# Kernel optimization log

Measured on AMD Instinct MI355X. Metric: run time of the kernel, lower is better.

Reference implementation:

```python
import jax, jax.numpy as jnp
import numpy as np

N_NODES = 100000
N_EDGES = 1600000
IN_DIM = 256
OUT_DIM = 64


def setup_inputs() -> dict:
    key = jax.random.key(0)
    k1, k2, k3 = jax.random.split(key, 3)
    inputs = jax.random.normal(k1, (N_NODES, IN_DIM), dtype=jnp.float32)
    edge_index = jax.random.randint(k2, (2, N_EDGES), 0, N_NODES, dtype=jnp.int64)
    # Xavier-uniform weight as in nn.init.xavier_uniform_
    limit = float(np.sqrt(6.0 / (IN_DIM + OUT_DIM)))
    weight = jax.random.uniform(k3, (IN_DIM, OUT_DIM), minval=-limit, maxval=limit, dtype=jnp.float32)
    return {"inputs": inputs, "edge_index": edge_index, "weight": weight}


def reference(inputs, edge_index, weight):
    # Dense projection: [N, out_dim]
    x = inputs @ weight
    # Sparse adjacency matmul: out[r] = sum_{(r,c) in edges} x[c]
    rows, cols = edge_index[0], edge_index[1]
    agg = jax.ops.segment_sum(x[cols], rows, num_segments=inputs.shape[0])
    return jax.nn.sigmoid(agg)
```

## Files before the change

### kernel.cpp

```cpp
#include <hip/hip_runtime.h>
#include <hip/hip_fp16.h>
#include <math.h>

#define N_NODES 100000
#define N_EDGES 1600000
#define IN_DIM 256
#define OUT_DIM 64

#define NB 256
#define RPB 391
#define BCAP 6912
#define CAP 32
#define CHUNK_E 2048
#define NBIN_BLK ((N_EDGES + CHUNK_E - 1) / CHUNK_E)

#define X_OFF         0UL
#define WIMG_OFF      25600000UL
#define OFFSETS_OFF   26000000UL
#define BCUR_OFF      26400016UL
#define SORTED_OFF    26801088UL

typedef short bf16x8 __attribute__((ext_vector_type(8)));
typedef float f32x4 __attribute__((ext_vector_type(4)));

__global__ __launch_bounds__(256) void convert_weight(const float* __restrict__ w,
                                                      ushort* __restrict__ img) {
    const int g = blockIdx.x * 256 + threadIdx.x;
    const int j = g & 7, l = (g >> 3) & 63, ts = g >> 9;
    const int s = ts & 7, t = ts >> 3;
    const int k = s * 32 + (l >> 4) * 8 + j;
    const int c = t * 16 + (l & 15);
    const float v = w[k * OUT_DIM + c];
    const unsigned b = __float_as_uint(v);
    const float r = v - __uint_as_float(b & 0xFFFF0000u);
    img[(ts * 2 + 0) * 512 + l * 8 + j] = (ushort)(b >> 16);
    img[(ts * 2 + 1) * 512 + l * 8 + j] = (ushort)(__float_as_uint(r) >> 16);
}

__global__ __launch_bounds__(256) void gemm_mfma(const float* __restrict__ inputs,
                                                 const ushort* __restrict__ wimg,
                                                 __half* __restrict__ x) {
    __shared__ ushort lds[32768];
    const int tid = threadIdx.x;

    #pragma unroll
    for (int i = 0; i < 16; ++i) {
        const int c = tid + i * 256;
        *(int4*)(lds + c * 8) = *(const int4*)(wimg + c * 8);
    }
    __syncthreads();

    const int wv = tid >> 6, l = tid & 63;
    const int rbase = blockIdx.x * 64 + wv * 16;
    const int arow_idx = rbase + (l & 15);
    const int row_c = arow_idx < N_NODES ? arow_idx : N_NODES - 1;
    const float* arow = inputs + (size_t)row_c * IN_DIM;
    const int koff = (l >> 4) * 8;

    bf16x8 ah[8], al[8];
    #pragma unroll
    for (int s = 0; s < 8; ++s) {
        const float4 p = *(const float4*)(arow + s * 32 + koff);
        const float4 q = *(const float4*)(arow + s * 32 + koff + 4);
        const float v[8] = {p.x, p.y, p.z, p.w, q.x, q.y, q.z, q.w};
        #pragma unroll
        for (int j = 0; j < 8; ++j) {
            const unsigned b = __float_as_uint(v[j]);
            const float r = v[j] - __uint_as_float(b & 0xFFFF0000u);
            ah[s][j] = (short)(b >> 16);
            al[s][j] = (short)(__float_as_uint(r) >> 16);
        }
    }

    f32x4 acc[4];
    #pragma unroll
    for (int t = 0; t < 4; ++t) acc[t] = (f32x4){0.f, 0.f, 0.f, 0.f};

    const bf16x8* b8 = (const bf16x8*)lds;
    #pragma unroll
    for (int t = 0; t < 4; ++t) {
        #pragma unroll
        for (int s = 0; s < 8; ++s) {
            const bf16x8 bh = b8[((t * 8 + s) * 2 + 0) * 64 + l];
            const bf16x8 blo = b8[((t * 8 + s) * 2 + 1) * 64 + l];
            acc[t] = __builtin_amdgcn_mfma_f32_16x16x32_bf16(ah[s], bh, acc[t], 0, 0, 0);
            acc[t] = __builtin_amdgcn_mfma_f32_16x16x32_bf16(al[s], bh, acc[t], 0, 0, 0);
            acc[t] = __builtin_amdgcn_mfma_f32_16x16x32_bf16(ah[s], blo, acc[t], 0, 0, 0);
        }
    }

    const int mbase = rbase + (l >> 4) * 4;
    #pragma unroll
    for (int reg = 0; reg < 4; ++reg) {
        const int row = mbase + reg;
        if (row < N_NODES) {
            #pragma unroll
            for (int t = 0; t < 4; ++t)
                x[(size_t)row * OUT_DIM + t * 16 + (l & 15)] = __float2half(acc[t][reg]);
        }
    }
}

__global__ __launch_bounds__(256) void bin_kernel(const int* __restrict__ rows,
                                                  const int* __restrict__ cols,
                                                  int* __restrict__ bcur,
                                                  int* __restrict__ bp) {
    __shared__ int lbuf[NB * CAP];
    __shared__ int lcnt[NB], ltot[NB], lbase[NB];
    const int tid = threadIdx.x;
    lcnt[tid] = 0;
    __syncthreads();

    const int base = blockIdx.x * CHUNK_E;
    #pragma unroll
    for (int g = 0; g < 2; ++g) {
        const int e = base + (g * 256 + tid) * 4;
        if (e < N_EDGES) {
            const int4 r4 = *(const int4*)(rows + e);
            const int4 c4 = *(const int4*)(cols + e);
            const int rr[4] = {r4.x, r4.y, r4.z, r4.w};
            const int cc[4] = {c4.x, c4.y, c4.z, c4.w};
            #pragma unroll
            for (int u = 0; u < 4; ++u) {
                const int r = rr[u];
                const int b = r / RPB;
                const int pack = ((r - b * RPB) << 17) | cc[u];
                const int p = atomicAdd(&lcnt[b], 1);
                if (p < CAP) {
                    lbuf[b * CAP + p] = pack;
                } else {
                    const int gp = atomicAdd(&bcur[b], 1);
                    bp[b * BCAP + gp] = pack;
                }
            }
        }
    }
    __syncthreads();
    {
        const int tot = min(lcnt[tid], CAP);
        ltot[tid] = tot;
        lbase[tid] = atomicAdd(&bcur[tid], tot);
    }
    __syncthreads();
    #pragma unroll
    for (int k = 0; k < 32; ++k) {
        const int b = (k << 3) + (tid >> 5);
        const int i = tid & 31;
        if (i < ltot[b]) bp[b * BCAP + lbase[b] + i] = lbuf[b * CAP + i];
    }
}

__global__ __launch_bounds__(256) void sort_kernel(const int* __restrict__ bp,
                                                   const int* __restrict__ bcur,
                                                   int* __restrict__ offsets,
                                                   int* __restrict__ sorted_cols) {
    __shared__ int ebuf[BCAP];
    __shared__ int sa[256], sb2[256];
    __shared__ int hist[512];
    __shared__ int cur[RPB + 1];
    const int b = blockIdx.x, t = threadIdx.x;

    sa[t] = bcur[t];
    hist[t] = 0; hist[t + 256] = 0;
    __syncthreads();

    int* src = sa; int* dst = sb2;
    for (int off = 1; off < 256; off <<= 1) {
        const int v = src[t] + ((t >= off) ? src[t - off] : 0);
        dst[t] = v; __syncthreads();
        int* tmp = src; src = dst; dst = tmp;
    }
    const int n = bcur[b];
    const int gbase = src[b] - n;
    const int bb = b * BCAP;

    int i = t;
    for (; i + 768 < n; i += 1024) {
        const int v0 = bp[bb + i], v1 = bp[bb + i + 256];
        const int v2 = bp[bb + i + 512], v3 = bp[bb + i + 768];
        ebuf[i] = v0; ebuf[i + 256] = v1; ebuf[i + 512] = v2; ebuf[i + 768] = v3;
        atomicAdd(&hist[v0 >> 17], 1);
        atomicAdd(&hist[v1 >> 17], 1);
        atomicAdd(&hist[v2 >> 17], 1);
        atomicAdd(&hist[v3 >> 17], 1);
    }
    for (; i < n; i += 256) {
        const int v = bp[bb + i];
        ebuf[i] = v;
        atomicAdd(&hist[v >> 17], 1);
    }
    __syncthreads();

    const int h0 = hist[2 * t], h1 = hist[2 * t + 1];
    const int sum2 = h0 + h1;
    sa[t] = sum2; __syncthreads();
    src = sa; dst = sb2;
    for (int off = 1; off < 256; off <<= 1) {
        const int v = src[t] + ((t >= off) ? src[t - off] : 0);
        dst[t] = v; __syncthreads();
        int* tmp = src; src = dst; dst = tmp;
    }
    const int S = src[t];
    const int e0 = 2 * t, e1 = 2 * t + 1;
    const int x0 = S - sum2;
    const int x1 = S - h1;
    if (e0 < RPB) {
        cur[e0] = x0;
        const int row = b * RPB + e0;
        if (row <= N_NODES) offsets[row] = gbase + x0;
    }
    if (e1 < RPB) {
        cur[e1] = x1;
        const int row = b * RPB + e1;
        if (row <= N_NODES) offsets[row] = gbase + x1;
    }
    __syncthreads();

    i = t;
    for (; i + 768 < n; i += 1024) {
        const int v0 = ebuf[i], v1 = ebuf[i + 256], v2 = ebuf[i + 512], v3 = ebuf[i + 768];
        const int p0 = atomicAdd(&cur[v0 >> 17], 1);
        const int p1 = atomicAdd(&cur[v1 >> 17], 1);
        const int p2 = atomicAdd(&cur[v2 >> 17], 1);
        const int p3 = atomicAdd(&cur[v3 >> 17], 1);
        sorted_cols[gbase + p0] = v0 & 0x1FFFF;
        sorted_cols[gbase + p1] = v1 & 0x1FFFF;
        sorted_cols[gbase + p2] = v2 & 0x1FFFF;
        sorted_cols[gbase + p3] = v3 & 0x1FFFF;
    }
    for (; i < n; i += 256) {
        const int v = ebuf[i];
        const int p = atomicAdd(&cur[v >> 17], 1);
        sorted_cols[gbase + p] = v & 0x1FFFF;
    }
}

__global__ __launch_bounds__(256) void aggregate_kernel(const int* __restrict__ offsets,
                                                        const int* __restrict__ sorted_cols,
                                                        const __half* __restrict__ x,
                                                        float* __restrict__ out) {
    const int row = blockIdx.x * 4 + (threadIdx.x >> 6);
    const int lane = threadIdx.x & 63;
    if (row >= N_NODES) return;
    const int start = offsets[row];
    const int end = offsets[row + 1];
    float acc = 0.f;
    int j = start;
    for (; j + 7 < end; j += 8) {
        int c[8];
        #pragma unroll
        for (int u = 0; u < 8; ++u) c[u] = sorted_cols[j + u];
        float a[8];
        #pragma unroll
        for (int u = 0; u < 8; ++u) a[u] = __half2float(x[(size_t)c[u] * OUT_DIM + lane]);
        acc += ((a[0] + a[1]) + (a[2] + a[3])) + ((a[4] + a[5]) + (a[6] + a[7]));
    }
    for (; j < end; ++j)
        acc += __half2float(x[(size_t)sorted_cols[j] * OUT_DIM + lane]);
    out[(size_t)row * OUT_DIM + lane] = 1.f / (1.f + __expf(-acc));
}

extern "C" void kernel_launch(void* const* d_in, const int* in_sizes, int n_in,
                              void* d_out, int out_size, void* d_ws, size_t ws_size,
                              hipStream_t stream) {
    const float* inputs = (const float*)d_in[0];
    const int* edge_index = (const int*)d_in[1];
    const float* weight = (const float*)d_in[2];
    float* out = (float*)d_out;

    char* ws = (char*)d_ws;
    __half* x        = (__half*)(ws + X_OFF);
    int* bp          = (int*)(ws + X_OFF);
    ushort* wimg     = (ushort*)(ws + WIMG_OFF);
    int* offsets     = (int*)(ws + OFFSETS_OFF);
    int* bcur        = (int*)(ws + BCUR_OFF);
    int* sorted_cols = (int*)(ws + SORTED_OFF);

    const int* rows = edge_index;
    const int* cols = edge_index + N_EDGES;

    hipMemsetAsync(bcur, 0, NB * sizeof(int), stream);

    bin_kernel<<<NBIN_BLK, 256, 0, stream>>>(rows, cols, bcur, bp);
    sort_kernel<<<NB, 256, 0, stream>>>(bp, bcur, offsets, sorted_cols);

    convert_weight<<<64, 256, 0, stream>>>(weight, wimg);
    gemm_mfma<<<(N_NODES + 63) / 64, 256, 0, stream>>>(inputs, wimg, x);

    aggregate_kernel<<<(N_NODES + 3) / 4, 256, 0, stream>>>(offsets, sorted_cols, x, out);
}
```

Before: 275.0 us.

## Drop per-row sort and aggregate bucketed edges with shared-memory atomics

Removes the counting-sort kernel and the CSR offsets. The aggregation now launches one block per row bucket. Each block gathers x rows for its bucket's edges and accumulates them into a shared-memory tile with float atomics, then applies the sigmoid and writes out with vector stores. Buckets are halved in size (512 buckets of 196 rows) and each bin block handles twice as many edges. This saves a full kernel launch and a pass over the edge list, at the cost of only 512 aggregation blocks with large LDS footprints and contended LDS atomics, which may cut the latency hiding for the random gathers.

```diff
diff --git a/kernel.cpp b/kernel.cpp
--- a/kernel.cpp
+++ b/kernel.cpp
@@ -7,18 +7,17 @@
 #define IN_DIM 256
 #define OUT_DIM 64
 
-#define NB 256
-#define RPB 391
-#define BCAP 6912
-#define CAP 32
-#define CHUNK_E 2048
+#define NB 512
+#define RPB 196
+#define BCAP 3712
+#define CAP 24
+#define CHUNK_E 4096
 #define NBIN_BLK ((N_EDGES + CHUNK_E - 1) / CHUNK_E)
 
 #define X_OFF         0UL
-#define WIMG_OFF      25600000UL
-#define OFFSETS_OFF   26000000UL
-#define BCUR_OFF      26400016UL
-#define SORTED_OFF    26801088UL
+#define BP_OFF        12800000UL
+#define WIMG_OFF      20500000UL
+#define BCUR_OFF      20600000UL
 
 typedef short bf16x8 __attribute__((ext_vector_type(8)));
 typedef float f32x4 __attribute__((ext_vector_type(4)));
@@ -108,12 +107,12 @@
     __shared__ int lbuf[NB * CAP];
     __shared__ int lcnt[NB], ltot[NB], lbase[NB];
     const int tid = threadIdx.x;
-    lcnt[tid] = 0;
+    lcnt[tid] = 0; lcnt[tid + 256] = 0;
     __syncthreads();
 
     const int base = blockIdx.x * CHUNK_E;
     #pragma unroll
-    for (int g = 0; g < 2; ++g) {
+    for (int g = 0; g < 4; ++g) {
         const int e = base + (g * 256 + tid) * 4;
         if (e < N_EDGES) {
             const int4 r4 = *(const int4*)(rows + e);
@@ -136,128 +135,65 @@
         }
     }
     __syncthreads();
-    {
-        const int tot = min(lcnt[tid], CAP);
-        ltot[tid] = tot;
-        lbase[tid] = atomicAdd(&bcur[tid], tot);
-    }
-    __syncthreads();
-    #pragma unroll
-    for (int k = 0; k < 32; ++k) {
+    #pragma unroll
+    for (int q = 0; q < 2; ++q) {
+        const int b = tid + q * 256;
+        const int tot = min(lcnt[b], CAP);
+        ltot[b] = tot;
+        lbase[b] = atomicAdd(&bcur[b], tot);
+    }
+    __syncthreads();
+    #pragma unroll
+    for (int k = 0; k < 64; ++k) {
         const int b = (k << 3) + (tid >> 5);
         const int i = tid & 31;
         if (i < ltot[b]) bp[b * BCAP + lbase[b] + i] = lbuf[b * CAP + i];
     }
 }
 
-__global__ __launch_bounds__(256) void sort_kernel(const int* __restrict__ bp,
-                                                   const int* __restrict__ bcur,
-                                                   int* __restrict__ offsets,
-                                                   int* __restrict__ sorted_cols) {
-    __shared__ int ebuf[BCAP];
-    __shared__ int sa[256], sb2[256];
-    __shared__ int hist[512];
-    __shared__ int cur[RPB + 1];
-    const int b = blockIdx.x, t = threadIdx.x;
-
-    sa[t] = bcur[t];
-    hist[t] = 0; hist[t + 256] = 0;
-    __syncthreads();
-
-    int* src = sa; int* dst = sb2;
-    for (int off = 1; off < 256; off <<= 1) {
-        const int v = src[t] + ((t >= off) ? src[t - off] : 0);
-        dst[t] = v; __syncthreads();
-        int* tmp = src; src = dst; dst = tmp;
-    }
-    const int n = bcur[b];
-    const int gbase = src[b] - n;
-    const int bb = b * BCAP;
-
-    int i = t;
-    for (; i + 768 < n; i += 1024) {
-        const int v0 = bp[bb + i], v1 = bp[bb + i + 256];
-        const int v2 = bp[bb + i + 512], v3 = bp[bb + i + 768];
-        ebuf[i] = v0; ebuf[i + 256] = v1; ebuf[i + 512] = v2; ebuf[i + 768] = v3;
-        atomicAdd(&hist[v0 >> 17], 1);
-        atomicAdd(&hist[v1 >> 17], 1);
-        atomicAdd(&hist[v2 >> 17], 1);
-        atomicAdd(&hist[v3 >> 17], 1);
-    }
-    for (; i < n; i += 256) {
-        const int v = bp[bb + i];
-        ebuf[i] = v;
-        atomicAdd(&hist[v >> 17], 1);
-    }
-    __syncthreads();
-
-    const int h0 = hist[2 * t], h1 = hist[2 * t + 1];
-    const int sum2 = h0 + h1;
-    sa[t] = sum2; __syncthreads();
-    src = sa; dst = sb2;
-    for (int off = 1; off < 256; off <<= 1) {
-        const int v = src[t] + ((t >= off) ? src[t - off] : 0);
-        dst[t] = v; __syncthreads();
-        int* tmp = src; src = dst; dst = tmp;
-    }
-    const int S = src[t];
-    const int e0 = 2 * t, e1 = 2 * t + 1;
-    const int x0 = S - sum2;
-    const int x1 = S - h1;
-    if (e0 < RPB) {
-        cur[e0] = x0;
-        const int row = b * RPB + e0;
-        if (row <= N_NODES) offsets[row] = gbase + x0;
-    }
-    if (e1 < RPB) {
-        cur[e1] = x1;
-        const int row = b * RPB + e1;
-        if (row <= N_NODES) offsets[row] = gbase + x1;
-    }
-    __syncthreads();
-
-    i = t;
-    for (; i + 768 < n; i += 1024) {
-        const int v0 = ebuf[i], v1 = ebuf[i + 256], v2 = ebuf[i + 512], v3 = ebuf[i + 768];
-        const int p0 = atomicAdd(&cur[v0 >> 17], 1);
-        const int p1 = atomicAdd(&cur[v1 >> 17], 1);
-        const int p2 = atomicAdd(&cur[v2 >> 17], 1);
-        const int p3 = atomicAdd(&cur[v3 >> 17], 1);
-        sorted_cols[gbase + p0] = v0 & 0x1FFFF;
-        sorted_cols[gbase + p1] = v1 & 0x1FFFF;
-        sorted_cols[gbase + p2] = v2 & 0x1FFFF;
-        sorted_cols[gbase + p3] = v3 & 0x1FFFF;
-    }
-    for (; i < n; i += 256) {
-        const int v = ebuf[i];
-        const int p = atomicAdd(&cur[v >> 17], 1);
-        sorted_cols[gbase + p] = v & 0x1FFFF;
-    }
-}
-
-__global__ __launch_bounds__(256) void aggregate_kernel(const int* __restrict__ offsets,
-                                                        const int* __restrict__ sorted_cols,
+__global__ __launch_bounds__(256) void aggregate_kernel(const int* __restrict__ bp,
+                                                        const int* __restrict__ bcur,
                                                         const __half* __restrict__ x,
                                                         float* __restrict__ out) {
-    const int row = blockIdx.x * 4 + (threadIdx.x >> 6);
-    const int lane = threadIdx.x & 63;
-    if (row >= N_NODES) return;
-    const int start = offsets[row];
-    const int end = offsets[row + 1];
-    float acc = 0.f;
-    int j = start;
-    for (; j + 7 < end; j += 8) {
-        int c[8];
+    __shared__ float acc[RPB * OUT_DIM];
+    const int b = blockIdx.x, tid = threadIdx.x;
+    const int w = tid >> 6, lane = tid & 63;
+
+    f32x4* a4 = (f32x4*)acc;
+    for (int i = tid; i < RPB * OUT_DIM / 4; i += 256) a4[i] = (f32x4){0.f, 0.f, 0.f, 0.f};
+    __syncthreads();
+
+    const int n = bcur[b];
+    const unsigned* bb = (const unsigned*)(bp + b * BCAP);
+
+    for (int j0 = w * 8; j0 < n; j0 += 32) {
         #pragma unroll
-        for (int u = 0; u < 8; ++u) c[u] = sorted_cols[j + u];
-        float a[8];
-        #pragma unroll
-        for (int u = 0; u < 8; ++u) a[u] = __half2float(x[(size_t)c[u] * OUT_DIM + lane]);
-        acc += ((a[0] + a[1]) + (a[2] + a[3])) + ((a[4] + a[5]) + (a[6] + a[7]));
-    }
-    for (; j < end; ++j)
-        acc += __half2float(x[(size_t)sorted_cols[j] * OUT_DIM + lane]);
-    out[(size_t)row * OUT_DIM + lane] = 1.f / (1.f + __expf(-acc));
+        for (int u = 0; u < 8; ++u) {
+            const int j = j0 + u;
+            if (j < n) {
+                const unsigned p = bb[j];
+                const int col = p & 0x1FFFF;
+                const int rl = p >> 17;
+                const float v = __half2float(x[(size_t)col * OUT_DIM + lane]);
+                atomicAdd(&acc[rl * OUT_DIM + lane], v);
+            }
+        }
+    }
+    __syncthreads();
+
+    for (int i = tid; i < RPB * (OUT_DIM / 4); i += 256) {
+        const int rr = i >> 4, q = i & 15;
+        const int row = b * RPB + rr;
+        if (row < N_NODES) {
+            const float* ap = acc + rr * OUT_DIM + q * 4;
+            float4 o;
+            o.x = 1.f / (1.f + __expf(-ap[0]));
+            o.y = 1.f / (1.f + __expf(-ap[1]));
+            o.z = 1.f / (1.f + __expf(-ap[2]));
+            o.w = 1.f / (1.f + __expf(-ap[3]));
+            *(float4*)(out + (size_t)row * OUT_DIM + q * 4) = o;
+        }
+    }
 }
 
 extern "C" void kernel_launch(void* const* d_in, const int* in_sizes, int n_in,
@@ -270,11 +206,9 @@
 
     char* ws = (char*)d_ws;
     __half* x        = (__half*)(ws + X_OFF);
-    int* bp          = (int*)(ws + X_OFF);
+    int* bp          = (int*)(ws + BP_OFF);
     ushort* wimg     = (ushort*)(ws + WIMG_OFF);
-    int* offsets     = (int*)(ws + OFFSETS_OFF);
     int* bcur        = (int*)(ws + BCUR_OFF);
-    int* sorted_cols = (int*)(ws + SORTED_OFF);
 
     const int* rows = edge_index;
     const int* cols = edge_index + N_EDGES;
@@ -282,10 +216,9 @@
     hipMemsetAsync(bcur, 0, NB * sizeof(int), stream);
 
     bin_kernel<<<NBIN_BLK, 256, 0, stream>>>(rows, cols, bcur, bp);
-    sort_kernel<<<NB, 256, 0, stream>>>(bp, bcur, offsets, sorted_cols);
 
     convert_weight<<<64, 256, 0, stream>>>(weight, wimg);
     gemm_mfma<<<(N_NODES + 63) / 64, 256, 0, stream>>>(inputs, wimg, x);
 
-    aggregate_kernel<<<(N_NODES + 3) / 4, 256, 0, stream>>>(offsets, sorted_cols, x, out);
-}
+    aggregate_kernel<<<NB, 256, 0, stream>>>(bp, bcur, x, out);
+}
```

Result: slower. 749.4 us (+172.5%).
